# Performance work log

Hardware: AMD Instinct MI355X
Metric: run time of the kernel (lower is better)

Reference implementation:

```python
import jax, jax.numpy as jnp
import numpy as np

EMBED = 1024

def setup_inputs() -> dict:
    key = jax.random.key(0)
    ks = jax.random.split(key, 10)
    s = 1.0 / np.sqrt(EMBED)
    inp = {
        "target": jax.random.normal(ks[0], (8, 2048, EMBED), dtype=jnp.float32),
        "source": jax.random.normal(ks[1], (8, 2048, EMBED), dtype=jnp.float32),
        "Wq": jax.random.uniform(ks[2], (EMBED, EMBED), jnp.float32, -s, s),
        "bq": jax.random.uniform(ks[3], (EMBED,), jnp.float32, -s, s),
        "Wk": jax.random.uniform(ks[4], (EMBED, EMBED), jnp.float32, -s, s),
        "bk": jax.random.uniform(ks[5], (EMBED,), jnp.float32, -s, s),
        "Wv": jax.random.uniform(ks[6], (EMBED, EMBED), jnp.float32, -s, s),
        "bv": jax.random.uniform(ks[7], (EMBED,), jnp.float32, -s, s),
        "Wo": jax.random.uniform(ks[8], (EMBED, EMBED), jnp.float32, -s, s),
        "bo": jax.random.uniform(ks[9], (EMBED,), jnp.float32, -s, s),
    }
    return inp

def reference(target, source, Wq, bq, Wk, bk, Wv, bv, Wo, bo):
    # Linear layers (torch Linear: x @ W.T + b)
    Q = jnp.einsum('btd,ed->bte', target, Wq) + bq   # [B, Tq, D]
    K = jnp.einsum('bsd,ed->bse', source, Wk) + bk   # [B, Tk, D]
    V = jnp.einsum('bsd,ed->bse', source, Wv) + bv   # [B, Tk, D]
    d_k = Q.shape[-1]
    scores = jnp.einsum('bte,bse->bts', Q, K) / jnp.sqrt(jnp.float32(d_k))  # [B, Tq, Tk]
    attn = jax.nn.softmax(scores, axis=-1)
    out = jnp.einsum('bts,bse->bte', attn, V)        # [B, Tq, D]
    return jnp.einsum('bte,oe->bto', out, Wo) + bo
```

## Files before the change

kernel.cpp:

```cpp
#include <hip/hip_runtime.h>
#include <stdint.h>

typedef unsigned short bf16_t;
typedef __attribute__((ext_vector_type(8))) short   short8;
typedef __attribute__((ext_vector_type(4))) float   floatx4;
typedef __attribute__((ext_vector_type(4))) unsigned int   uint4v;
typedef __attribute__((ext_vector_type(4))) unsigned short ushort4v;

#define GAS __attribute__((address_space(1)))
#define LAS __attribute__((address_space(3)))

__device__ __forceinline__ unsigned short f2bf(float f) {
  unsigned u = __float_as_uint(f);
  u += 0x7FFFu + ((u >> 16) & 1u);
  return (unsigned short)(u >> 16);
}
__device__ __forceinline__ void store_out(float* p, float v) { *p = v; }
__device__ __forceinline__ void store_out(bf16_t* p, float v) { *p = f2bf(v); }

__device__ __forceinline__ void g2l16(const bf16_t* g, bf16_t* l) {
  __builtin_amdgcn_global_load_lds((const GAS uint32_t*)g, (LAS uint32_t*)l, 16, 0, 0);
}

__global__ __launch_bounds__(256) void conv_f32_bf16(const float* __restrict__ s,
                                                     bf16_t* __restrict__ d) {
  size_t i = ((size_t)blockIdx.x * 256 + threadIdx.x) * 4;
  float4 v = *(const float4*)(s + i);
  ushort4v o = { f2bf(v.x), f2bf(v.y), f2bf(v.z), f2bf(v.w) };
  *(ushort4v*)(d + i) = o;
}

__global__ __launch_bounds__(256) void conv_w(const float* __restrict__ w0, const float* __restrict__ w1,
                                              const float* __restrict__ w2, const float* __restrict__ w3,
                                              bf16_t* __restrict__ d) {
  const float* s = blockIdx.y == 0 ? w0 : blockIdx.y == 1 ? w1 : blockIdx.y == 2 ? w2 : w3;
  size_t i = ((size_t)blockIdx.x * 256 + threadIdx.x) * 4;
  float4 v = *(const float4*)(s + i);
  ushort4v o = { f2bf(v.x), f2bf(v.y), f2bf(v.z), f2bf(v.w) };
  *(ushort4v*)(d + (size_t)blockIdx.y * 1048576 + i) = o;
}

template <typename OutT>
__global__ __launch_bounds__(256) void gemm_bt(
    const bf16_t* __restrict__ A, const bf16_t* __restrict__ B,
    const float* __restrict__ bias, OutT* __restrict__ C,
    int M, int N, int K, long aBat, long bBat, long cBat, float scale)
{
  const int tid  = threadIdx.x;
  const int lane = tid & 63;
  const int wv   = tid >> 6;

  int bx, by;
  {
    const int gx = gridDim.x, gy = gridDim.y;
    const int flat = blockIdx.y * gx + blockIdx.x;
    if ((gy & 7) == 0) {
      const int xcd = flat & 7;
      const int r   = flat >> 3;
      bx = r % gx;
      by = xcd + 8 * (r / gx);
    } else { bx = blockIdx.x; by = blockIdx.y; }
  }
  const int bm = by * 128;
  const int bn = bx * 128;
  A += (size_t)blockIdx.z * aBat;
  B += (size_t)blockIdx.z * bBat;
  C += (size_t)blockIdx.z * cBat;

  __shared__ bf16_t As[128 * 64];
  __shared__ bf16_t Bs[128 * 64];

  const int wm = (wv >> 1) * 64;
  const int wn = (wv & 1) * 64;

  floatx4 zero = {0.0f, 0.0f, 0.0f, 0.0f};
  floatx4 acc[4][4];
#pragma unroll
  for (int i = 0; i < 4; i++)
#pragma unroll
    for (int j = 0; j < 4; j++) acc[i][j] = zero;

  const int r8 = lane >> 3;
  const int sq = (((lane & 7) - r8) & 7) * 8;
  const bf16_t* gA = A + (size_t)(bm + wv * 32 + r8) * K + sq;
  const bf16_t* gB = B + (size_t)(bn + wv * 32 + r8) * K + sq;
  bf16_t* lA = As + wv * 2048 + lane * 8;
  bf16_t* lB = Bs + wv * 2048 + lane * 8;

  const int fr = lane & 15;
  const int kq = lane >> 4;
  const int frow  = fr * 64;
  const int slot0 = (((kq     + (fr & 7)) & 7) << 3);
  const int slot1 = (((kq + 4 + (fr & 7)) & 7) << 3);

  const int sA = (wv >> 1) * 4;
  const int sB = (wv & 1) * 4;

  for (int k0 = 0; k0 < K; k0 += 64) {
#pragma unroll
    for (int i = 0; i < 4; i++) {
      g2l16(gA + (size_t)(i * 8) * K, lA + i * 512);
      g2l16(gB + (size_t)(i * 8) * K, lB + i * 512);
    }
    gA += 64; gB += 64;
    __syncthreads();

    {
      short8 af[4], bfr[4];
#pragma unroll
      for (int i = 0; i < 4; i++)
        af[i] = *(const short8*)(As + (sA + i) * 1024 + frow + slot0);
#pragma unroll
      for (int i = 0; i < 4; i++)
        bfr[i] = *(const short8*)(Bs + (sB + i) * 1024 + frow + slot0);
#pragma unroll
      for (int mi = 0; mi < 4; mi++)
#pragma unroll
        for (int ni = 0; ni < 4; ni++)
          acc[mi][ni] = __builtin_amdgcn_mfma_f32_16x16x32_bf16(af[mi], bfr[ni], acc[mi][ni], 0, 0, 0);
    }
    {
      short8 af[4], bfr[4];
#pragma unroll
      for (int i = 0; i < 4; i++)
        af[i] = *(const short8*)(As + (sA + i) * 1024 + frow + slot1);
#pragma unroll
      for (int i = 0; i < 4; i++)
        bfr[i] = *(const short8*)(Bs + (sB + i) * 1024 + frow + slot1);
#pragma unroll
      for (int mi = 0; mi < 4; mi++)
#pragma unroll
        for (int ni = 0; ni < 4; ni++)
          acc[mi][ni] = __builtin_amdgcn_mfma_f32_16x16x32_bf16(af[mi], bfr[ni], acc[mi][ni], 0, 0, 0);
    }
    __syncthreads();
  }

  const int er = (lane >> 4) * 4;
  const int ec = lane & 15;
#pragma unroll
  for (int ni = 0; ni < 4; ni++) {
    const int col = bn + wn + ni * 16 + ec;
    const float bval = bias ? bias[col] : 0.0f;
#pragma unroll
    for (int mi = 0; mi < 4; mi++) {
      const int row0 = bm + wm + mi * 16 + er;
#pragma unroll
      for (int r = 0; r < 4; r++) {
        float v = (acc[mi][ni][r] + bval) * scale;
        store_out(C + (size_t)(row0 + r) * N + col, v);
      }
    }
  }
}

__global__ __launch_bounds__(256) void softmax_rows(bf16_t* __restrict__ S) {
  const int tid = threadIdx.x;
  bf16_t* row = S + (size_t)blockIdx.x * 2048;
  uint4v raw = *(const uint4v*)(row + tid * 8);
  float x[8];
#pragma unroll
  for (int j = 0; j < 4; j++) {
    unsigned w = raw[j];
    x[2 * j]     = __uint_as_float(w << 16);
    x[2 * j + 1] = __uint_as_float(w & 0xFFFF0000u);
  }
  float m = -1e30f;
#pragma unroll
  for (int j = 0; j < 8; j++) m = fmaxf(m, x[j]);
  for (int o = 32; o > 0; o >>= 1) m = fmaxf(m, __shfl_xor(m, o, 64));
  __shared__ float red[4];
  if ((tid & 63) == 0) red[tid >> 6] = m;
  __syncthreads();
  m = fmaxf(fmaxf(red[0], red[1]), fmaxf(red[2], red[3]));

  float e[8];
  float s = 0.0f;
#pragma unroll
  for (int j = 0; j < 8; j++) { e[j] = __expf(x[j] - m); s += e[j]; }
  for (int o = 32; o > 0; o >>= 1) s += __shfl_xor(s, o, 64);
  __syncthreads();
  if ((tid & 63) == 0) red[tid >> 6] = s;
  __syncthreads();
  s = red[0] + red[1] + red[2] + red[3];
  float inv = 1.0f / s;

  uint4v o4;
#pragma unroll
  for (int j = 0; j < 4; j++) {
    unsigned lo = f2bf(e[2 * j] * inv);
    unsigned hi = f2bf(e[2 * j + 1] * inv);
    o4[j] = lo | (hi << 16);
  }
  *(uint4v*)(row + tid * 8) = o4;
}

__global__ __launch_bounds__(256) void transpose64(const bf16_t* __restrict__ V,
                                                   bf16_t* __restrict__ Vt) {
  __shared__ bf16_t t[64][72];
  const int tid = threadIdx.x;
  const int e0 = blockIdx.x * 64;
  const int s0 = blockIdx.y * 64;
  const size_t bb = (size_t)blockIdx.z * (2048 * 1024);
  const int r = tid >> 2;
  const int c = (tid & 3) * 16;
  const bf16_t* src = V + bb + (size_t)(s0 + r) * 1024 + e0 + c;
  uint4v v0 = *(const uint4v*)src;
  uint4v v1 = *(const uint4v*)(src + 8);
  *(uint4v*)&t[r][c]     = v0;
  *(uint4v*)&t[r][c + 8] = v1;
  __syncthreads();
  __attribute__((aligned(16))) bf16_t vals[16];
#pragma unroll
  for (int j = 0; j < 16; j++) vals[j] = t[c + j][r];
  bf16_t* dst = Vt + bb + (size_t)(e0 + r) * 2048 + s0 + c;
  *(uint4v*)dst       = *(const uint4v*)vals;
  *(uint4v*)(dst + 8) = *(const uint4v*)(vals + 8);
}

extern "C" void kernel_launch(void* const* d_in, const int* in_sizes, int n_in,
                              void* d_out, int out_size, void* d_ws, size_t ws_size,
                              hipStream_t stream) {
  const float* target = (const float*)d_in[0];
  const float* source = (const float*)d_in[1];
  const float* Wq = (const float*)d_in[2];
  const float* bq = (const float*)d_in[3];
  const float* Wk = (const float*)d_in[4];
  const float* bk = (const float*)d_in[5];
  const float* Wv = (const float*)d_in[6];
  const float* bv = (const float*)d_in[7];
  const float* Wo = (const float*)d_in[8];
  const float* bo = (const float*)d_in[9];
  float* out = (float*)d_out;

  char* ws = (char*)d_ws;
  bf16_t* Qb  = (bf16_t*)(ws + 0);
  bf16_t* Kb  = (bf16_t*)(ws + 33554432);
  bf16_t* Vt  = (bf16_t*)(ws + 67108864);
  bf16_t* Wb  = (bf16_t*)(ws + 100663296);
  bf16_t* Tb  = (bf16_t*)(ws + 109051904);
  bf16_t* Sb  = Tb;
  bf16_t* Srb = (bf16_t*)(ws + 142606336);
  bf16_t* Vb  = (bf16_t*)(ws + 176160768);
  bf16_t* AO  = Vb;

  conv_f32_bf16<<<16384, 256, 0, stream>>>(target, Tb);
  conv_f32_bf16<<<16384, 256, 0, stream>>>(source, Srb);
  conv_w<<<dim3(1024, 4), 256, 0, stream>>>(Wq, Wk, Wv, Wo, Wb);

  gemm_bt<<<dim3(8, 128, 1), 256, 0, stream>>>(Tb,  Wb,           bq, Qb, 16384, 1024, 1024, 0L, 0L, 0L, 0.03125f);
  gemm_bt<<<dim3(8, 128, 1), 256, 0, stream>>>(Srb, Wb + 1048576, bk, Kb, 16384, 1024, 1024, 0L, 0L, 0L, 1.0f);
  gemm_bt<<<dim3(8, 128, 1), 256, 0, stream>>>(Srb, Wb + 2097152, bv, Vb, 16384, 1024, 1024, 0L, 0L, 0L, 1.0f);

  transpose64<<<dim3(16, 32, 8), 256, 0, stream>>>(Vb, Vt);

  gemm_bt<<<dim3(16, 16, 8), 256, 0, stream>>>(Qb, Kb, (const float*)nullptr, Sb,
      2048, 2048, 1024, (long)2048 * 1024, (long)2048 * 1024, (long)2048 * 2048, 1.0f);

  softmax_rows<<<16384, 256, 0, stream>>>(Sb);

  gemm_bt<<<dim3(8, 16, 8), 256, 0, stream>>>(Sb, Vt, (const float*)nullptr, AO,
      2048, 1024, 2048, (long)2048 * 2048, (long)1024 * 2048, (long)2048 * 1024, 1.0f);

  gemm_bt<<<dim3(8, 128, 1), 256, 0, stream>>>(AO, Wb + 3145728, bo, out,
      16384, 1024, 1024, 0L, 0L, 0L, 1.0f);
}
```

Baseline: 577.4 us.

## Replace 128x128 GEMM with double-buffered 256x256 8-wave pipelined GEMM

Rewrites the shared GEMM kernel to use 256x256 output tiles with 512 threads (8 waves), 128 KB of LDS split into double-buffered K halves, and prefetch of the next tile via global_load_lds interleaved with MFMA phases using explicit barriers and setprio. It also applies a new XCD-aware flat block remap across all grid dimensions and an XOR LDS swizzle. The intent is to raise arithmetic intensity and overlap global loads with compute, at the cost of more registers (128 accumulator floats per lane), fewer blocks per grid and reduced occupancy.

New measurement: 559.7 us. 1.03x faster.

```diff
diff --git a/kernel.cpp b/kernel.cpp
--- a/kernel.cpp
+++ b/kernel.cpp
@@ -41,7 +41,7 @@
 }
 
 template <typename OutT>
-__global__ __launch_bounds__(256) void gemm_bt(
+__global__ __launch_bounds__(512, 2) void gemm256(
     const bf16_t* __restrict__ A, const bf16_t* __restrict__ B,
     const float* __restrict__ bias, OutT* __restrict__ C,
     int M, int N, int K, long aBat, long bBat, long cBat, float scale)
@@ -50,104 +50,160 @@
   const int lane = tid & 63;
   const int wv   = tid >> 6;
 
-  int bx, by;
+  int bx, by, bz;
   {
-    const int gx = gridDim.x, gy = gridDim.y;
-    const int flat = blockIdx.y * gx + blockIdx.x;
-    if ((gy & 7) == 0) {
-      const int xcd = flat & 7;
-      const int r   = flat >> 3;
-      bx = r % gx;
-      by = xcd + 8 * (r / gx);
-    } else { bx = blockIdx.x; by = blockIdx.y; }
-  }
-  const int bm = by * 128;
-  const int bn = bx * 128;
-  A += (size_t)blockIdx.z * aBat;
-  B += (size_t)blockIdx.z * bBat;
-  C += (size_t)blockIdx.z * cBat;
-
-  __shared__ bf16_t As[128 * 64];
-  __shared__ bf16_t Bs[128 * 64];
-
-  const int wm = (wv >> 1) * 64;
-  const int wn = (wv & 1) * 64;
-
-  floatx4 zero = {0.0f, 0.0f, 0.0f, 0.0f};
-  floatx4 acc[4][4];
-#pragma unroll
-  for (int i = 0; i < 4; i++)
-#pragma unroll
-    for (int j = 0; j < 4; j++) acc[i][j] = zero;
-
-  const int r8 = lane >> 3;
-  const int sq = (((lane & 7) - r8) & 7) * 8;
-  const bf16_t* gA = A + (size_t)(bm + wv * 32 + r8) * K + sq;
-  const bf16_t* gB = B + (size_t)(bn + wv * 32 + r8) * K + sq;
-  bf16_t* lA = As + wv * 2048 + lane * 8;
-  bf16_t* lB = Bs + wv * 2048 + lane * 8;
+    const int gx = gridDim.x, gy = gridDim.y, gz = gridDim.z;
+    const int nwg = gx * gy * gz;
+    int flat = (blockIdx.z * gy + blockIdx.y) * gx + blockIdx.x;
+    if ((nwg & 7) == 0) {
+      const int q = nwg >> 3;
+      flat = (flat & 7) * q + (flat >> 3);
+    }
+    bx = flat % gx;
+    const int rem = flat / gx;
+    by = rem % gy;
+    bz = rem / gy;
+  }
+  const int bm = by * 256;
+  const int bn = bx * 256;
+  A += (size_t)bz * aBat;
+  B += (size_t)bz * bBat;
+  C += (size_t)bz * cBat;
+
+  __shared__ bf16_t sm[65536];
+
+  const int nt = K >> 6;
+
+  const int wm = (wv >> 2) * 128;
+  const int wn = (wv & 3) * 64;
 
   const int fr = lane & 15;
   const int kq = lane >> 4;
-  const int frow  = fr * 64;
-  const int slot0 = (((kq     + (fr & 7)) & 7) << 3);
-  const int slot1 = (((kq + 4 + (fr & 7)) & 7) << 3);
-
-  const int sA = (wv >> 1) * 4;
-  const int sB = (wv & 1) * 4;
-
-  for (int k0 = 0; k0 < K; k0 += 64) {
-#pragma unroll
-    for (int i = 0; i < 4; i++) {
-      g2l16(gA + (size_t)(i * 8) * K, lA + i * 512);
-      g2l16(gB + (size_t)(i * 8) * K, lB + i * 512);
-    }
-    gA += 64; gB += 64;
-    __syncthreads();
-
-    {
-      short8 af[4], bfr[4];
-#pragma unroll
-      for (int i = 0; i < 4; i++)
-        af[i] = *(const short8*)(As + (sA + i) * 1024 + frow + slot0);
-#pragma unroll
-      for (int i = 0; i < 4; i++)
-        bfr[i] = *(const short8*)(Bs + (sB + i) * 1024 + frow + slot0);
-#pragma unroll
-      for (int mi = 0; mi < 4; mi++)
-#pragma unroll
-        for (int ni = 0; ni < 4; ni++)
-          acc[mi][ni] = __builtin_amdgcn_mfma_f32_16x16x32_bf16(af[mi], bfr[ni], acc[mi][ni], 0, 0, 0);
-    }
-    {
-      short8 af[4], bfr[4];
-#pragma unroll
-      for (int i = 0; i < 4; i++)
-        af[i] = *(const short8*)(As + (sA + i) * 1024 + frow + slot1);
-#pragma unroll
-      for (int i = 0; i < 4; i++)
-        bfr[i] = *(const short8*)(Bs + (sB + i) * 1024 + frow + slot1);
-#pragma unroll
-      for (int mi = 0; mi < 4; mi++)
-#pragma unroll
-        for (int ni = 0; ni < 4; ni++)
-          acc[mi][ni] = __builtin_amdgcn_mfma_f32_16x16x32_bf16(af[mi], bfr[ni], acc[mi][ni], 0, 0, 0);
-    }
-    __syncthreads();
-  }
+  const int chE = kq ^ ((fr >> 1) & 3);
+  const unsigned fA = (unsigned)((wm + fr) * 32 + chE * 8);
+  const unsigned fB = (unsigned)((wn + fr) * 32 + chE * 8);
+
+  const unsigned c0    = (unsigned)((tid & 3) ^ ((tid >> 3) & 3));
+  const unsigned soff  = (unsigned)((tid >> 2) * K + c0 * 8);
+  const unsigned kx128 = (unsigned)(K << 7);
+  const unsigned lOff  = (unsigned)(wv * 512 + lane * 8);
+
+  const bf16_t* gA = A + (size_t)bm * K;
+  const bf16_t* gB = B + (size_t)bn * K;
+
+#define SMA(b, kh) (sm + (((b) << 1) | (kh)) * 8192)
+#define SMB(b, kh) (sm + 32768 + (((b) << 1) | (kh)) * 8192)
+#define STG(gbase, lbase)                                   \
+  do {                                                      \
+    g2l16((gbase) + soff,         (lbase) + lOff);          \
+    g2l16((gbase) + soff + kx128, (lbase) + lOff + 4096);   \
+  } while (0)
+
+  floatx4 acc[8][4];
+  floatx4 zero = {0.0f, 0.0f, 0.0f, 0.0f};
+#pragma unroll
+  for (int i = 0; i < 8; i++)
+#pragma unroll
+    for (int j = 0; j < 4; j++) acc[i][j] = zero;
+
+  STG(gA,      SMA(0, 0));
+  STG(gB,      SMB(0, 0));
+  STG(gA + 32, SMA(0, 1));
+  STG(gB + 32, SMB(0, 1));
+  if (nt > 1) {
+    STG(gA + 64, SMA(1, 0));
+    STG(gB + 64, SMB(1, 0));
+    asm volatile("s_waitcnt vmcnt(4)" ::: "memory");
+  } else {
+    asm volatile("s_waitcnt vmcnt(0)" ::: "memory");
+  }
+  asm volatile("s_barrier" ::: "memory");
+
+  int cur = 0;
+  for (int t = 0; t < nt; ++t) {
+    const int kc = t << 6;
+    short8 a_[4], b_[4];
+    const bf16_t* Ac0 = SMA(cur, 0);
+    const bf16_t* Ac1 = SMA(cur, 1);
+    const bf16_t* Bc0 = SMB(cur, 0);
+    const bf16_t* Bc1 = SMB(cur, 1);
+
+#pragma unroll
+    for (int i = 0; i < 4; i++) a_[i] = *(const short8*)(Ac0 + fA + i * 512);
+#pragma unroll
+    for (int i = 0; i < 4; i++) b_[i] = *(const short8*)(Bc0 + fB + i * 512);
+    if (t + 1 < nt) STG(gA + kc + 96, SMA(cur ^ 1, 1));
+    asm volatile("s_barrier" ::: "memory");
+    __builtin_amdgcn_s_setprio(1);
+#pragma unroll
+    for (int mi = 0; mi < 4; mi++)
+#pragma unroll
+      for (int ni = 0; ni < 4; ni++)
+        acc[mi][ni] = __builtin_amdgcn_mfma_f32_16x16x32_bf16(a_[mi], b_[ni], acc[mi][ni], 0, 0, 0);
+    __builtin_amdgcn_s_setprio(0);
+    asm volatile("s_barrier" ::: "memory");
+
+#pragma unroll
+    for (int i = 0; i < 4; i++) a_[i] = *(const short8*)(Ac0 + fA + (4 + i) * 512);
+    if (t + 1 < nt) STG(gB + kc + 96, SMB(cur ^ 1, 1));
+    asm volatile("s_barrier" ::: "memory");
+    __builtin_amdgcn_s_setprio(1);
+#pragma unroll
+    for (int mi = 0; mi < 4; mi++)
+#pragma unroll
+      for (int ni = 0; ni < 4; ni++)
+        acc[4 + mi][ni] = __builtin_amdgcn_mfma_f32_16x16x32_bf16(a_[mi], b_[ni], acc[4 + mi][ni], 0, 0, 0);
+    __builtin_amdgcn_s_setprio(0);
+    asm volatile("s_barrier" ::: "memory");
+
+#pragma unroll
+    for (int i = 0; i < 4; i++) a_[i] = *(const short8*)(Ac1 + fA + i * 512);
+#pragma unroll
+    for (int i = 0; i < 4; i++) b_[i] = *(const short8*)(Bc1 + fB + i * 512);
+    if (t + 2 < nt) STG(gA + kc + 128, SMA(cur, 0));
+    asm volatile("s_barrier" ::: "memory");
+    __builtin_amdgcn_s_setprio(1);
+#pragma unroll
+    for (int mi = 0; mi < 4; mi++)
+#pragma unroll
+      for (int ni = 0; ni < 4; ni++)
+        acc[mi][ni] = __builtin_amdgcn_mfma_f32_16x16x32_bf16(a_[mi], b_[ni], acc[mi][ni], 0, 0, 0);
+    __builtin_amdgcn_s_setprio(0);
+    asm volatile("s_barrier" ::: "memory");
+
+#pragma unroll
+    for (int i = 0; i < 4; i++) a_[i] = *(const short8*)(Ac1 + fA + (4 + i) * 512);
+    if (t + 2 < nt) STG(gB + kc + 128, SMB(cur, 0));
+    asm volatile("s_barrier" ::: "memory");
+    __builtin_amdgcn_s_setprio(1);
+#pragma unroll
+    for (int mi = 0; mi < 4; mi++)
+#pragma unroll
+      for (int ni = 0; ni < 4; ni++)
+        acc[4 + mi][ni] = __builtin_amdgcn_mfma_f32_16x16x32_bf16(a_[mi], b_[ni], acc[4 + mi][ni], 0, 0, 0);
+    __builtin_amdgcn_s_setprio(0);
+    if (t + 2 < nt) asm volatile("s_waitcnt vmcnt(4)" ::: "memory");
+    else            asm volatile("s_waitcnt vmcnt(0)" ::: "memory");
+    asm volatile("s_barrier" ::: "memory");
+
+    cur ^= 1;
+  }
+#undef STG
+#undef SMB
+#undef SMA
 
   const int er = (lane >> 4) * 4;
   const int ec = lane & 15;
 #pragma unroll
-  for (int ni = 0; ni < 4; ni++) {
-    const int col = bn + wn + ni * 16 + ec;
+  for (int nf = 0; nf < 4; nf++) {
+    const int col = bn + wn + nf * 16 + ec;
     const float bval = bias ? bias[col] : 0.0f;
 #pragma unroll
-    for (int mi = 0; mi < 4; mi++) {
-      const int row0 = bm + wm + mi * 16 + er;
+    for (int mf = 0; mf < 8; mf++) {
+      const int row0 = bm + wm + mf * 16 + er;
 #pragma unroll
       for (int r = 0; r < 4; r++) {
-        float v = (acc[mi][ni][r] + bval) * scale;
+        float v = (acc[mf][nf][r] + bval) * scale;
         store_out(C + (size_t)(row0 + r) * N + col, v);
       }
     }
@@ -248,20 +304,20 @@
   conv_f32_bf16<<<16384, 256, 0, stream>>>(source, Srb);
   conv_w<<<dim3(1024, 4), 256, 0, stream>>>(Wq, Wk, Wv, Wo, Wb);
 
-  gemm_bt<<<dim3(8, 128, 1), 256, 0, stream>>>(Tb,  Wb,           bq, Qb, 16384, 1024, 1024, 0L, 0L, 0L, 0.03125f);
-  gemm_bt<<<dim3(8, 128, 1), 256, 0, stream>>>(Srb, Wb + 1048576, bk, Kb, 16384, 1024, 1024, 0L, 0L, 0L, 1.0f);
-  gemm_bt<<<dim3(8, 128, 1), 256, 0, stream>>>(Srb, Wb + 2097152, bv, Vb, 16384, 1024, 1024, 0L, 0L, 0L, 1.0f);
+  gemm256<<<dim3(4, 64, 1), 512, 0, stream>>>(Tb,  Wb,           bq, Qb, 16384, 1024, 1024, 0L, 0L, 0L, 0.03125f);
+  gemm256<<<dim3(4, 64, 1), 512, 0, stream>>>(Srb, Wb + 1048576, bk, Kb, 16384, 1024, 1024, 0L, 0L, 0L, 1.0f);
+  gemm256<<<dim3(4, 64, 1), 512, 0, stream>>>(Srb, Wb + 2097152, bv, Vb, 16384, 1024, 1024, 0L, 0L, 0L, 1.0f);
 
   transpose64<<<dim3(16, 32, 8), 256, 0, stream>>>(Vb, Vt);
 
-  gemm_bt<<<dim3(16, 16, 8), 256, 0, stream>>>(Qb, Kb, (const float*)nullptr, Sb,
+  gemm256<<<dim3(8, 8, 8), 512, 0, stream>>>(Qb, Kb, (const float*)nullptr, Sb,
       2048, 2048, 1024, (long)2048 * 1024, (long)2048 * 1024, (long)2048 * 2048, 1.0f);
 
   softmax_rows<<<16384, 256, 0, stream>>>(Sb);
 
-  gemm_bt<<<dim3(8, 16, 8), 256, 0, stream>>>(Sb, Vt, (const float*)nullptr, AO,
+  gemm256<<<dim3(4, 8, 8), 512, 0, stream>>>(Sb, Vt, (const float*)nullptr, AO,
       2048, 1024, 2048, (long)2048 * 2048, (long)1024 * 2048, (long)2048 * 1024, 1.0f);
 
-  gemm_bt<<<dim3(8, 128, 1), 256, 0, stream>>>(AO, Wb + 3145728, bo, out,
+  gemm256<<<dim3(4, 64, 1), 512, 0, stream>>>(AO, Wb + 3145728, bo, out,
       16384, 1024, 1024, 0L, 0L, 0L, 1.0f);
 }
```
